# Optimization experiments

Measured on AMD Instinct MI355X. Metric: run time of the kernel, lower is better.

Reference implementation:

```python
import jax, jax.numpy as jnp
import numpy as np
from jax import lax

VOCAB, E, H, B, T, NCLS = 50000, 1024, 1024, 1024, 64, 2

def setup_inputs() -> dict:
    key = jax.random.key(0)
    ks = jax.random.split(key, 10)
    s = 0.05
    return {
        "x": jax.random.randint(ks[0], (B, T), 0, VOCAB),
        "emb": jax.random.normal(ks[1], (VOCAB, E), jnp.float32) * s,
        "W_ih": jax.random.normal(ks[2], (4 * H, E), jnp.float32) * s,
        "W_hh": jax.random.normal(ks[3], (4 * H, H), jnp.float32) * s,
        "b_ih": jax.random.normal(ks[4], (4 * H,), jnp.float32) * s,
        "b_hh": jax.random.normal(ks[5], (4 * H,), jnp.float32) * s,
        "W_out": jax.random.normal(ks[6], (NCLS, H), jnp.float32) * s,
        "b_out": jax.random.normal(ks[7], (NCLS,), jnp.float32) * s,
        "h0": jax.random.normal(ks[8], (B, H), jnp.float32),
        "c0": jax.random.normal(ks[9], (B, H), jnp.float32),
    }

def reference(x, emb, W_ih, W_hh, b_ih, b_hh, W_out, b_out, h0, c0):
    # Embedding lookup then transpose to time-major, like x.transpose(1, 0)
    xe = emb[x]                      # [B, T, E]
    xt = jnp.swapaxes(xe, 0, 1)      # [T, B, E]

    def step(carry, xi):
        h, c = carry
        # nn.LSTMCell: gates in (i, f, g, o) order
        gates = xi @ W_ih.T + b_ih + h @ W_hh.T + b_hh  # [B, 4H]
        i, f, g, o = jnp.split(gates, 4, axis=-1)
        c2 = jax.nn.sigmoid(f) * c + jax.nn.sigmoid(i) * jnp.tanh(g)
        h2 = jax.nn.sigmoid(o) * jnp.tanh(c2)
        # Per-step classifier on cell state c (as in the original loop)
        logp = jax.nn.log_softmax(c2 @ W_out.T + b_out, axis=-1)
        return (h2, c2), logp

    (hT, cT), actions_pair = lax.scan(step, (h0, c0), xt)  # actions_pair: [T, B, NCLS]
    out_final = cT @ W_out.T + b_out                       # linear on last cell state
    return actions_pair, out_final
```

## Files before the change

### kernel.cpp

```cpp
#include <hip/hip_runtime.h>

typedef __bf16 bf16x8 __attribute__((ext_vector_type(8)));
typedef float f32x4 __attribute__((ext_vector_type(4)));
typedef unsigned short u16;
typedef unsigned int u32;

#define T_ 64
#define B_ 1024
#define H_ 1024
#define G4_ 4096
#define HB_ (B_ * H_)
#define CHUNK_ 16
#define NBLK_ 512
#define PARTSZ_ (B_ * 2 * 64)

__device__ inline u16 f2bf(float f) {
  u32 u = __float_as_uint(f);
  u32 r = (u + 0x7fffu + ((u >> 16) & 1u)) >> 16;
  return (u16)r;
}

__device__ inline uint2 cvt4(float4 v) {
  uint2 r;
  r.x = (u32)f2bf(v.x) | ((u32)f2bf(v.y) << 16);
  r.y = (u32)f2bf(v.z) | ((u32)f2bf(v.w) << 16);
  return r;
}

__device__ __forceinline__ void gload16(const void* g, void* l) {
  __builtin_amdgcn_global_load_lds(
      (const __attribute__((address_space(1))) unsigned int*)g,
      (__attribute__((address_space(3))) unsigned int*)l, 16, 0, 0);
}

__device__ __forceinline__ void gload16_nt(const void* g, void* l) {
  __builtin_amdgcn_global_load_lds(
      (const __attribute__((address_space(1))) unsigned int*)g,
      (__attribute__((address_space(3))) unsigned int*)l, 16, 0, 2);
}

__device__ __forceinline__ void store_wt16(u16* p, u16 v) {
  asm volatile("global_store_short %0, %1, off sc0 sc1" :: "v"(p), "v"((u32)v) : "memory");
}

__device__ inline float fsig(float x) { return 1.f / (1.f + __expf(-x)); }
__device__ inline float ftanh(float x) {
  float e = __expf(2.f * x);
  return 1.f - 2.f / (e + 1.f);
}

__global__ void prep_kernel(const float* __restrict__ W_ih, const float* __restrict__ W_hh,
                            const float* __restrict__ b_ih, const float* __restrict__ b_hh,
                            const float* __restrict__ h0,
                            u16* __restrict__ WihP, u16* __restrict__ WhhP,
                            float* __restrict__ bcP, u16* __restrict__ h0slot,
                            u32* __restrict__ flags) {
  int bid = blockIdx.x, tid = threadIdx.x;
  if (bid < 4096) {
    int np = bid;
    int gate = (np >> 4) & 3;
    int j = ((np >> 6) << 4) | (np & 15);
    size_t srow = (size_t)(gate * 1024 + j) * 1024;
    int base = tid << 2;
    *(uint2*)(WihP + (size_t)np * 1024 + base) = cvt4(*(const float4*)(W_ih + srow + base));
    *(uint2*)(WhhP + (size_t)np * 1024 + base) = cvt4(*(const float4*)(W_hh + srow + base));
  } else if (bid < 5120) {
    int i = ((bid - 4096) * 256 + tid) << 2;
    *(uint2*)(h0slot + i) = cvt4(*(const float4*)(h0 + i));
  } else if (bid == 5120) {
#pragma unroll
    for (int q = 0; q < 16; ++q) {
      int np = q * 256 + tid;
      int gate = (np >> 4) & 3;
      int j = ((np >> 6) << 4) | (np & 15);
      int srcn = gate * 1024 + j;
      bcP[np] = b_ih[srcn] + b_hh[srcn];
    }
  } else {
    int idx = ((bid - 5121) * 256 + tid) << 2;
    *(uint4*)(flags + idx) = uint4{0u, 0u, 0u, 0u};
  }
}

__global__ void gather_kernel(const int* __restrict__ x, const float* __restrict__ emb,
                              u16* __restrict__ XEall) {
  int b = blockIdx.x, tc = blockIdx.y;
  int row = x[b * T_ + tc];
  int e = threadIdx.x << 2;
  float4 v = *(const float4*)(emb + (size_t)row * H_ + e);
  *(uint2*)(XEall + ((size_t)tc * B_ + b) * H_ + e) = cvt4(v);
}

__global__ void __launch_bounds__(256, 2) xproj_kernel(
    const u16* __restrict__ XEc, const u16* __restrict__ WihP,
    const float* __restrict__ bcP, u16* __restrict__ GXc) {
  __shared__ char smem[32768];
  const int tid = threadIdx.x;
  const int lane = tid & 63;
  const int wave = tid >> 6;
  const int wm = wave >> 1, wn = wave & 1;
  const int hbid = blockIdx.x;
  const int xcd = hbid & 7;
  const int s9 = hbid >> 3;
  const int mg = s9 >> 7;
  const int rem = s9 & 127;
  const int n0 = (rem >> 2) * 128;
  const int m0 = (xcd * 16 + mg * 4 + (rem & 3)) * 128;

  const u16* srcA[4];
  const u16* srcB[4];
  int betaA[4], betaB[4];
#pragma unroll
  for (int s = 0; s < 4; ++s) {
    int beta = (s * 256 + tid) * 16;
    int row = beta >> 7;
    int colu = (beta & 127) ^ ((row & 7) << 4);
    int kl = colu >> 1;
    srcA[s] = XEc + (size_t)(m0 + row) * 1024 + kl;
    srcB[s] = WihP + (size_t)(n0 + row) * 1024 + kl;
    betaA[s] = beta;
    betaB[s] = 16384 + beta;
  }

  f32x4 acc[4][4] = {};
  const int rsel = lane & 15;
  const int ksel = (lane >> 4) << 4;

  for (int kt = 0; kt < 16; ++kt) {
#pragma unroll
    for (int s = 0; s < 4; ++s) gload16(srcA[s], smem + betaA[s]);
#pragma unroll
    for (int s = 0; s < 4; ++s) gload16(srcB[s], smem + betaB[s]);
#pragma unroll
    for (int s = 0; s < 4; ++s) { srcA[s] += 64; srcB[s] += 64; }
    __syncthreads();
#pragma unroll
    for (int kk = 0; kk < 2; ++kk) {
      const int colb = kk * 64 + ksel;
      bf16x8 af[4], bfr[4];
#pragma unroll
      for (int mi = 0; mi < 4; ++mi) {
        int row = wm * 64 + mi * 16 + rsel;
        af[mi] = *(const bf16x8*)(smem + row * 128 + (colb ^ ((row & 7) << 4)));
      }
#pragma unroll
      for (int ni = 0; ni < 4; ++ni) {
        int row = wn * 64 + ni * 16 + rsel;
        bfr[ni] = *(const bf16x8*)(smem + 16384 + row * 128 + (colb ^ ((row & 7) << 4)));
      }
#pragma unroll
      for (int mi = 0; mi < 4; ++mi)
#pragma unroll
        for (int ni = 0; ni < 4; ++ni)
          acc[mi][ni] = __builtin_amdgcn_mfma_f32_16x16x32_bf16(af[mi], bfr[ni], acc[mi][ni], 0, 0, 0);
    }
    __syncthreads();
  }

  const int rbase = (lane >> 4) << 2;
  const int cbase = lane & 15;
  float bc[4];
#pragma unroll
  for (int ni = 0; ni < 4; ++ni) bc[ni] = bcP[n0 + wn * 64 + ni * 16 + cbase];
#pragma unroll
  for (int mi = 0; mi < 4; ++mi) {
#pragma unroll
    for (int ni = 0; ni < 4; ++ni) {
      int gc = n0 + wn * 64 + ni * 16 + cbase;
#pragma unroll
      for (int r = 0; r < 4; ++r) {
        int gm = m0 + wm * 64 + mi * 16 + rbase + r;
        GXc[(size_t)gm * G4_ + gc] = f2bf(acc[mi][ni][r] + bc[ni]);
      }
    }
  }
}

__global__ void __launch_bounds__(512, 4) rec_kernel(
    const u16* __restrict__ h0slot, u16* __restrict__ hring,
    const u16* __restrict__ WhhP, const u16* __restrict__ GXall,
    const float* __restrict__ c0, float* __restrict__ partAll,
    const float* __restrict__ Wout, u32* __restrict__ flags) {
  __shared__ char smem[81920];
  const int tid = threadIdx.x;
  const int lane = tid & 63;
  const int qm = tid >> 6;
  const int hbid = blockIdx.x;
  const int L = (hbid & 7) * 64 + (hbid >> 3);
  const int bx = L >> 3;
  const int by = L & 7;
  const int n0 = bx * 64;
  const int m0 = by * 128;

  int offA[2], offGX[2], betaS[2];
  int offB, betaB;
#pragma unroll
  for (int s = 0; s < 2; ++s) {
    int beta = (s * 512 + tid) * 16;
    int row = beta >> 7;
    int colu = (beta & 127) ^ ((row & 7) << 4);
    offA[s] = (m0 + row) * 1024 + (colu >> 1);
    offGX[s] = (m0 + row) * G4_ + n0 + (colu >> 1);
    betaS[s] = beta;
  }
  {
    int beta = tid * 16;
    int row = beta >> 7;
    int colu = (beta & 127) ^ ((row & 7) << 4);
    offB = (n0 + row) * 1024 + (colu >> 1);
    betaB = beta;
  }

  const int rsel = lane & 15;
  const int ksel = (lane >> 4) << 4;
  const int rbase = (lane >> 4) << 2;
  const int cbase = lane & 15;
  const int j = bx * 16 + cbase;
  const float w0 = Wout[j], w1 = Wout[1024 + j];

  float creg[4];
#pragma unroll
  for (int r = 0; r < 4; ++r)
    creg[r] = c0[(size_t)(m0 + qm * 16 + rbase + r) * H_ + j];

#pragma unroll
  for (int s = 0; s < 2; ++s) gload16_nt(GXall + offGX[s], smem + 49152 + betaS[s]);

#pragma unroll 1
  for (int t = 0; t < T_; ++t) {
    gload16(WhhP + offB, smem + 32768 + betaB);

    if (t) {
      if (tid < 64) {
        const u32* fg = flags + (size_t)(t - 1) * NBLK_ + by * 64;
        int guard = 0;
        while (true) {
          u32 v = __hip_atomic_load(fg + tid, __ATOMIC_RELAXED, __HIP_MEMORY_SCOPE_AGENT);
          if (__all(v != 0)) break;
          __builtin_amdgcn_s_sleep(4);
          if (++guard > (1 << 18)) break;
        }
      }
      __syncthreads();
    }

    const u16* hbR = t ? (hring + (size_t)(t - 1) * HB_) : h0slot;
    u16* hbW = hring + (size_t)t * HB_;

#pragma unroll
    for (int s = 0; s < 2; ++s) gload16(hbR + offA[s], smem + betaS[s]);

    f32x4 acc[4] = {};
#pragma unroll
    for (int kt = 0; kt < 16; ++kt) {
      const int cur = kt & 1;
      const int abase = cur * 16384;
      const int bbase = 32768 + cur * 8192;
      if (kt < 15) {
        const int nab = (cur ^ 1) * 16384;
        const int nbb = 32768 + (cur ^ 1) * 8192;
        const int kadv = (kt + 1) * 64;
#pragma unroll
        for (int s = 0; s < 2; ++s) gload16(hbR + offA[s] + kadv, smem + nab + betaS[s]);
        gload16(WhhP + offB + kadv, smem + nbb + betaB);
        asm volatile("s_waitcnt vmcnt(3)" ::: "memory");
      } else {
        asm volatile("s_waitcnt vmcnt(0)" ::: "memory");
      }
      __builtin_amdgcn_s_barrier();
      __builtin_amdgcn_sched_barrier(0);
#pragma unroll
      for (int kk = 0; kk < 2; ++kk) {
        const int colb = kk * 64 + ksel;
        bf16x8 af, bfr[4];
        {
          int row = qm * 16 + rsel;
          af = *(const bf16x8*)(smem + abase + row * 128 + (colb ^ ((row & 7) << 4)));
        }
#pragma unroll
        for (int ni = 0; ni < 4; ++ni) {
          int row = ni * 16 + rsel;
          bfr[ni] = *(const bf16x8*)(smem + bbase + row * 128 + (colb ^ ((row & 7) << 4)));
        }
#pragma unroll
        for (int ni = 0; ni < 4; ++ni)
          acc[ni] = __builtin_amdgcn_mfma_f32_16x16x32_bf16(af, bfr[ni], acc[ni], 0, 0, 0);
      }
      __builtin_amdgcn_s_barrier();
      __builtin_amdgcn_sched_barrier(0);
    }

    const char* lsGX = smem + 49152 + (t & 1) * 16384;
#pragma unroll
    for (int r = 0; r < 4; ++r) {
      int grow = qm * 16 + rbase + r;
      int b = m0 + grow;
      int gxswz = (grow & 7) << 4;
      float gx0 = __uint_as_float(
          (u32)*(const u16*)(lsGX + ((grow << 7) | ((cbase << 1) ^ gxswz))) << 16);
      float gx1 = __uint_as_float(
          (u32)*(const u16*)(lsGX + ((grow << 7) | ((((16 + cbase) << 1)) ^ gxswz))) << 16);
      float gx2 = __uint_as_float(
          (u32)*(const u16*)(lsGX + ((grow << 7) | ((((32 + cbase) << 1)) ^ gxswz))) << 16);
      float gx3 = __uint_as_float(
          (u32)*(const u16*)(lsGX + ((grow << 7) | ((((48 + cbase) << 1)) ^ gxswz))) << 16);
      float gi = acc[0][r] + gx0;
      float gf = acc[1][r] + gx1;
      float gg = acc[2][r] + gx2;
      float go = acc[3][r] + gx3;
      float c2 = fsig(gf) * creg[r] + fsig(gi) * ftanh(gg);
      float h2 = fsig(go) * ftanh(c2);
      creg[r] = c2;
      store_wt16(hbW + (size_t)b * H_ + j, f2bf(h2));
    }

    if (t + 1 < T_) {
      const u16* GXn = GXall + (size_t)(t + 1) * B_ * G4_;
      const int gxb = 49152 + ((t + 1) & 1) * 16384;
#pragma unroll
      for (int s = 0; s < 2; ++s) gload16_nt(GXn + offGX[s], smem + gxb + betaS[s]);
      asm volatile("s_waitcnt vmcnt(2)" ::: "memory");
    } else {
      asm volatile("s_waitcnt vmcnt(0)" ::: "memory");
    }
    __syncthreads();
    if (tid == 0)
      __hip_atomic_store(flags + (size_t)t * NBLK_ + by * 64 + bx, 1u,
                         __ATOMIC_RELAXED, __HIP_MEMORY_SCOPE_AGENT);

    float* partW = partAll + (size_t)t * PARTSZ_;
#pragma unroll
    for (int r = 0; r < 4; ++r) {
      int b = m0 + qm * 16 + rbase + r;
      float p0 = creg[r] * w0, p1 = creg[r] * w1;
#pragma unroll
      for (int off = 1; off < 16; off <<= 1) {
        p0 += __shfl_xor(p0, off);
        p1 += __shfl_xor(p1, off);
      }
      if (cbase == 0) {
        partW[(b << 7) + bx] = p0;
        partW[(b << 7) + 64 + bx] = p1;
      }
    }
  }
}

__global__ void final_kernel(const float* __restrict__ partAll, const float* __restrict__ bout,
                             float* __restrict__ out) {
  int gid = blockIdx.x * 256 + threadIdx.x;
  int t = gid >> 11;
  int r = gid & 2047;
  int b = r >> 1, cls = r & 1;
  const float4* pp = (const float4*)(partAll + (size_t)t * PARTSZ_ + (b << 7) + cls * 64);
  float4 sv = {0.f, 0.f, 0.f, 0.f};
#pragma unroll
  for (int q = 0; q < 16; ++q) {
    float4 v = pp[q];
    sv.x += v.x; sv.y += v.y; sv.z += v.z; sv.w += v.w;
  }
  float l = sv.x + sv.y + sv.z + sv.w + bout[cls];
  float other = __shfl_xor(l, 1);
  float m = fmaxf(l, other);
  float ls = m + __logf(__expf(l - m) + __expf(other - m));
  out[(size_t)t * (B_ * 2) + b * 2 + cls] = l - ls;
  if (t == 63) out[(size_t)T_ * (B_ * 2) + b * 2 + cls] = l;
}

extern "C" void kernel_launch(void* const* d_in, const int* in_sizes, int n_in,
                              void* d_out, int out_size, void* d_ws, size_t ws_size,
                              hipStream_t stream) {
  const int* x      = (const int*)d_in[0];
  const float* emb  = (const float*)d_in[1];
  const float* W_ih = (const float*)d_in[2];
  const float* W_hh = (const float*)d_in[3];
  const float* b_ih = (const float*)d_in[4];
  const float* b_hh = (const float*)d_in[5];
  const float* W_out = (const float*)d_in[6];
  const float* b_out = (const float*)d_in[7];
  const float* h0   = (const float*)d_in[8];
  const float* c0   = (const float*)d_in[9];
  float* out = (float*)d_out;

  char* w = (char*)d_ws;
  u16* WihP = (u16*)w;   w += (size_t)G4_ * H_ * 2;
  u16* WhhP = (u16*)w;   w += (size_t)G4_ * H_ * 2;
  u16* XEall = (u16*)w;  w += (size_t)T_ * HB_ * 2;
  u16* GXall = (u16*)w;  w += (size_t)T_ * B_ * G4_ * 2;
  u16* h0slot = (u16*)w; w += (size_t)HB_ * 2;
  float* bcP = (float*)w;     w += (size_t)G4_ * 4;
  float* partAll = (float*)w; w += (size_t)T_ * PARTSZ_ * 4;
  u32* flags = (u32*)w;       w += (size_t)T_ * NBLK_ * 4;

  prep_kernel<<<5153, 256, 0, stream>>>(W_ih, W_hh, b_ih, b_hh, h0,
                                        WihP, WhhP, bcP, h0slot, flags);
  gather_kernel<<<dim3(B_, T_), 256, 0, stream>>>(x, emb, XEall);
  for (int ch = 0; ch < T_ / CHUNK_; ++ch) {
    xproj_kernel<<<4096, 256, 0, stream>>>(XEall + (size_t)ch * CHUNK_ * HB_, WihP, bcP,
                                           GXall + (size_t)ch * CHUNK_ * B_ * G4_);
  }
  rec_kernel<<<NBLK_, 512, 0, stream>>>(h0slot, XEall , WhhP, GXall, c0,
                                        partAll, W_out, flags);
  final_kernel<<<512, 256, 0, stream>>>(partAll, b_out, out);
}
```

Before: 1.593 ms.

## Fuse input projection into recurrent kernel, computing next-step gates in LDS

Removes the separate chunked input-projection GEMM and its large bf16 gate buffer in global memory. Each recurrent block now computes its slice of the next timestep's input gates from the embeddings and W_ih into shared memory, after publishing its step flag, so the work can overlap the cross-block wait. A dedicated h ring buffer replaces the reuse of the embedding buffer. This trades global memory traffic and extra launches for more per-step compute inside the latency-bound recurrence loop.

```diff
diff --git a/kernel.cpp b/kernel.cpp
--- a/kernel.cpp
+++ b/kernel.cpp
@@ -10,7 +10,6 @@
 #define H_ 1024
 #define G4_ 4096
 #define HB_ (B_ * H_)
-#define CHUNK_ 16
 #define NBLK_ 512
 #define PARTSZ_ (B_ * 2 * 64)
 
@@ -31,12 +30,6 @@
   __builtin_amdgcn_global_load_lds(
       (const __attribute__((address_space(1))) unsigned int*)g,
       (__attribute__((address_space(3))) unsigned int*)l, 16, 0, 0);
-}
-
-__device__ __forceinline__ void gload16_nt(const void* g, void* l) {
-  __builtin_amdgcn_global_load_lds(
-      (const __attribute__((address_space(1))) unsigned int*)g,
-      (__attribute__((address_space(3))) unsigned int*)l, 16, 0, 2);
 }
 
 __device__ __forceinline__ void store_wt16(u16* p, u16 v) {
@@ -91,95 +84,67 @@
   *(uint2*)(XEall + ((size_t)tc * B_ + b) * H_ + e) = cvt4(v);
 }
 
-__global__ void __launch_bounds__(256, 2) xproj_kernel(
-    const u16* __restrict__ XEc, const u16* __restrict__ WihP,
-    const float* __restrict__ bcP, u16* __restrict__ GXc) {
-  __shared__ char smem[32768];
-  const int tid = threadIdx.x;
-  const int lane = tid & 63;
-  const int wave = tid >> 6;
-  const int wm = wave >> 1, wn = wave & 1;
-  const int hbid = blockIdx.x;
-  const int xcd = hbid & 7;
-  const int s9 = hbid >> 3;
-  const int mg = s9 >> 7;
-  const int rem = s9 & 127;
-  const int n0 = (rem >> 2) * 128;
-  const int m0 = (xcd * 16 + mg * 4 + (rem & 3)) * 128;
-
-  const u16* srcA[4];
-  const u16* srcB[4];
-  int betaA[4], betaB[4];
-#pragma unroll
-  for (int s = 0; s < 4; ++s) {
-    int beta = (s * 256 + tid) * 16;
-    int row = beta >> 7;
-    int colu = (beta & 127) ^ ((row & 7) << 4);
-    int kl = colu >> 1;
-    srcA[s] = XEc + (size_t)(m0 + row) * 1024 + kl;
-    srcB[s] = WihP + (size_t)(n0 + row) * 1024 + kl;
-    betaA[s] = beta;
-    betaB[s] = 16384 + beta;
-  }
-
-  f32x4 acc[4][4] = {};
-  const int rsel = lane & 15;
-  const int ksel = (lane >> 4) << 4;
-
-  for (int kt = 0; kt < 16; ++kt) {
-#pragma unroll
-    for (int s = 0; s < 4; ++s) gload16(srcA[s], smem + betaA[s]);
-#pragma unroll
-    for (int s = 0; s < 4; ++s) gload16(srcB[s], smem + betaB[s]);
-#pragma unroll
-    for (int s = 0; s < 4; ++s) { srcA[s] += 64; srcB[s] += 64; }
-    __syncthreads();
-#pragma unroll
-    for (int kk = 0; kk < 2; ++kk) {
-      const int colb = kk * 64 + ksel;
-      bf16x8 af[4], bfr[4];
-#pragma unroll
-      for (int mi = 0; mi < 4; ++mi) {
-        int row = wm * 64 + mi * 16 + rsel;
-        af[mi] = *(const bf16x8*)(smem + row * 128 + (colb ^ ((row & 7) << 4)));
-      }
-#pragma unroll
-      for (int ni = 0; ni < 4; ++ni) {
-        int row = wn * 64 + ni * 16 + rsel;
-        bfr[ni] = *(const bf16x8*)(smem + 16384 + row * 128 + (colb ^ ((row & 7) << 4)));
-      }
-#pragma unroll
-      for (int mi = 0; mi < 4; ++mi)
-#pragma unroll
-        for (int ni = 0; ni < 4; ++ni)
-          acc[mi][ni] = __builtin_amdgcn_mfma_f32_16x16x32_bf16(af[mi], bfr[ni], acc[mi][ni], 0, 0, 0);
-    }
-    __syncthreads();
-  }
-
-  const int rbase = (lane >> 4) << 2;
-  const int cbase = lane & 15;
-  float bc[4];
-#pragma unroll
-  for (int ni = 0; ni < 4; ++ni) bc[ni] = bcP[n0 + wn * 64 + ni * 16 + cbase];
-#pragma unroll
-  for (int mi = 0; mi < 4; ++mi) {
-#pragma unroll
-    for (int ni = 0; ni < 4; ++ni) {
-      int gc = n0 + wn * 64 + ni * 16 + cbase;
-#pragma unroll
-      for (int r = 0; r < 4; ++r) {
-        int gm = m0 + wm * 64 + mi * 16 + rbase + r;
-        GXc[(size_t)gm * G4_ + gc] = f2bf(acc[mi][ni][r] + bc[ni]);
-      }
-    }
-  }
-}
+#define XPROJ_PHASE(XEt, gxOff) do {                                          \
+    _Pragma("unroll")                                                         \
+    for (int s = 0; s < 2; ++s) gload16((XEt) + offA[s], smem + betaS[s]);    \
+    gload16(WihP + offB, smem + 32768 + betaB);                               \
+    f32x4 acc2[4] = {};                                                       \
+    _Pragma("unroll")                                                         \
+    for (int kt = 0; kt < 16; ++kt) {                                         \
+      const int cur = kt & 1;                                                 \
+      const int abase = cur * 16384;                                          \
+      const int bbase = 32768 + cur * 8192;                                   \
+      if (kt < 15) {                                                          \
+        const int nab = (cur ^ 1) * 16384;                                    \
+        const int nbb = 32768 + (cur ^ 1) * 8192;                             \
+        const int kadv = (kt + 1) * 64;                                       \
+        _Pragma("unroll")                                                     \
+        for (int s = 0; s < 2; ++s)                                           \
+          gload16((XEt) + offA[s] + kadv, smem + nab + betaS[s]);             \
+        gload16(WihP + offB + kadv, smem + nbb + betaB);                      \
+        asm volatile("s_waitcnt vmcnt(3)" ::: "memory");                      \
+      } else {                                                                \
+        asm volatile("s_waitcnt vmcnt(0)" ::: "memory");                      \
+      }                                                                       \
+      __builtin_amdgcn_s_barrier();                                           \
+      __builtin_amdgcn_sched_barrier(0);                                      \
+      _Pragma("unroll")                                                       \
+      for (int kk = 0; kk < 2; ++kk) {                                        \
+        const int colb = kk * 64 + ksel;                                      \
+        bf16x8 af, bfr[4];                                                    \
+        {                                                                     \
+          int row = qm * 16 + rsel;                                           \
+          af = *(const bf16x8*)(smem + abase + row * 128 + (colb ^ ((row & 7) << 4))); \
+        }                                                                     \
+        _Pragma("unroll")                                                     \
+        for (int ni = 0; ni < 4; ++ni) {                                      \
+          int row = ni * 16 + rsel;                                           \
+          bfr[ni] = *(const bf16x8*)(smem + bbase + row * 128 + (colb ^ ((row & 7) << 4))); \
+        }                                                                     \
+        _Pragma("unroll")                                                     \
+        for (int ni = 0; ni < 4; ++ni)                                        \
+          acc2[ni] = __builtin_amdgcn_mfma_f32_16x16x32_bf16(af, bfr[ni], acc2[ni], 0, 0, 0); \
+      }                                                                       \
+      __builtin_amdgcn_s_barrier();                                           \
+      __builtin_amdgcn_sched_barrier(0);                                      \
+    }                                                                         \
+    _Pragma("unroll")                                                         \
+    for (int ni = 0; ni < 4; ++ni) {                                          \
+      _Pragma("unroll")                                                       \
+      for (int r2 = 0; r2 < 4; ++r2) {                                        \
+        int grow = qm * 16 + rbase + r2;                                      \
+        int col = ni * 16 + cbase;                                            \
+        *(u16*)(smem + (gxOff) + ((grow << 7) | ((col << 1) ^ ((grow & 7) << 4)))) = \
+            f2bf(acc2[ni][r2] + bc4[ni]);                                     \
+      }                                                                       \
+    }                                                                         \
+  } while (0)
 
 __global__ void __launch_bounds__(512, 4) rec_kernel(
     const u16* __restrict__ h0slot, u16* __restrict__ hring,
-    const u16* __restrict__ WhhP, const u16* __restrict__ GXall,
-    const float* __restrict__ c0, float* __restrict__ partAll,
+    const u16* __restrict__ WhhP, const u16* __restrict__ WihP,
+    const u16* __restrict__ XEall, const float* __restrict__ c0,
+    const float* __restrict__ bcP, float* __restrict__ partAll,
     const float* __restrict__ Wout, u32* __restrict__ flags) {
   __shared__ char smem[81920];
   const int tid = threadIdx.x;
@@ -192,7 +157,7 @@
   const int n0 = bx * 64;
   const int m0 = by * 128;
 
-  int offA[2], offGX[2], betaS[2];
+  int offA[2], betaS[2];
   int offB, betaB;
 #pragma unroll
   for (int s = 0; s < 2; ++s) {
@@ -200,7 +165,6 @@
     int row = beta >> 7;
     int colu = (beta & 127) ^ ((row & 7) << 4);
     offA[s] = (m0 + row) * 1024 + (colu >> 1);
-    offGX[s] = (m0 + row) * G4_ + n0 + (colu >> 1);
     betaS[s] = beta;
   }
   {
@@ -217,14 +181,16 @@
   const int cbase = lane & 15;
   const int j = bx * 16 + cbase;
   const float w0 = Wout[j], w1 = Wout[1024 + j];
+  float bc4[4];
+#pragma unroll
+  for (int ni = 0; ni < 4; ++ni) bc4[ni] = bcP[n0 + ni * 16 + cbase];
 
   float creg[4];
 #pragma unroll
   for (int r = 0; r < 4; ++r)
     creg[r] = c0[(size_t)(m0 + qm * 16 + rbase + r) * H_ + j];
 
-#pragma unroll
-  for (int s = 0; s < 2; ++s) gload16_nt(GXall + offGX[s], smem + 49152 + betaS[s]);
+  XPROJ_PHASE(XEall, 49152);
 
 #pragma unroll 1
   for (int t = 0; t < T_; ++t) {
@@ -241,8 +207,8 @@
           if (++guard > (1 << 18)) break;
         }
       }
-      __syncthreads();
-    }
+    }
+    __syncthreads();
 
     const u16* hbR = t ? (hring + (size_t)(t - 1) * HB_) : h0slot;
     u16* hbW = hring + (size_t)t * HB_;
@@ -314,15 +280,7 @@
       store_wt16(hbW + (size_t)b * H_ + j, f2bf(h2));
     }
 
-    if (t + 1 < T_) {
-      const u16* GXn = GXall + (size_t)(t + 1) * B_ * G4_;
-      const int gxb = 49152 + ((t + 1) & 1) * 16384;
-#pragma unroll
-      for (int s = 0; s < 2; ++s) gload16_nt(GXn + offGX[s], smem + gxb + betaS[s]);
-      asm volatile("s_waitcnt vmcnt(2)" ::: "memory");
-    } else {
-      asm volatile("s_waitcnt vmcnt(0)" ::: "memory");
-    }
+    asm volatile("s_waitcnt vmcnt(0)" ::: "memory");
     __syncthreads();
     if (tid == 0)
       __hip_atomic_store(flags + (size_t)t * NBLK_ + by * 64 + bx, 1u,
@@ -342,6 +300,12 @@
         partW[(b << 7) + bx] = p0;
         partW[(b << 7) + 64 + bx] = p1;
       }
+    }
+
+    if (t + 1 < T_) {
+      const u16* XEn = XEall + (size_t)(t + 1) * HB_;
+      const int gxOff = 49152 + ((t + 1) & 1) * 16384;
+      XPROJ_PHASE(XEn, gxOff);
     }
   }
 }
@@ -386,7 +350,7 @@
   u16* WihP = (u16*)w;   w += (size_t)G4_ * H_ * 2;
   u16* WhhP = (u16*)w;   w += (size_t)G4_ * H_ * 2;
   u16* XEall = (u16*)w;  w += (size_t)T_ * HB_ * 2;
-  u16* GXall = (u16*)w;  w += (size_t)T_ * B_ * G4_ * 2;
+  u16* hring = (u16*)w;  w += (size_t)T_ * HB_ * 2;
   u16* h0slot = (u16*)w; w += (size_t)HB_ * 2;
   float* bcP = (float*)w;     w += (size_t)G4_ * 4;
   float* partAll = (float*)w; w += (size_t)T_ * PARTSZ_ * 4;
@@ -395,11 +359,7 @@
   prep_kernel<<<5153, 256, 0, stream>>>(W_ih, W_hh, b_ih, b_hh, h0,
                                         WihP, WhhP, bcP, h0slot, flags);
   gather_kernel<<<dim3(B_, T_), 256, 0, stream>>>(x, emb, XEall);
-  for (int ch = 0; ch < T_ / CHUNK_; ++ch) {
-    xproj_kernel<<<4096, 256, 0, stream>>>(XEall + (size_t)ch * CHUNK_ * HB_, WihP, bcP,
-                                           GXall + (size_t)ch * CHUNK_ * B_ * G4_);
-  }
-  rec_kernel<<<NBLK_, 512, 0, stream>>>(h0slot, XEall , WhhP, GXall, c0,
+  rec_kernel<<<NBLK_, 512, 0, stream>>>(h0slot, hring, WhhP, WihP, XEall, c0, bcP,
                                         partAll, W_out, flags);
   final_kernel<<<512, 256, 0, stream>>>(partAll, b_out, out);
 }
```

Result: slower. 2.028 ms (+27.3%).
